# Kernel tuning notes

Hardware: AMD Instinct MI355X
Metric: run time of the kernel (lower is better)

## Reference

```python
import math
import jax, jax.numpy as jnp
import numpy as np

jax.config.update("jax_enable_x64", True)  # original module computes attention in float64

MIN_NORM = 1e-08
B, S, G = 2, 2048, 16
D_MODEL, NHEAD = 512, 8
KDIM, VDIM = 512, 512
EK, EV = KDIM // NHEAD, VDIM // NHEAD
PARAM_SCALE = 0.02  # keep exp() in range; torch.randn params at this width would overflow exp


def setup_inputs() -> dict:
    key = jax.random.key(0)
    ks = jax.random.split(key, 9)
    f32 = jnp.float32
    return {
        "query": jax.random.normal(ks[0], (B, S, D_MODEL), f32),
        "key": jax.random.normal(ks[1], (B, S, D_MODEL), f32),
        "value": jax.random.normal(ks[2], (B, S, D_MODEL), f32),
        "context": jax.random.normal(ks[3], (B, G, D_MODEL), f32),
        "query_proj": jax.random.normal(ks[4], (1, D_MODEL, KDIM), f32) * PARAM_SCALE,
        "key_proj": jax.random.normal(ks[5], (1, D_MODEL, KDIM), f32) * PARAM_SCALE,
        "value_proj": jax.random.normal(ks[6], (1, D_MODEL, VDIM), f32) * PARAM_SCALE,
        "output_proj": jax.random.normal(ks[7], (1, VDIM, D_MODEL), f32) * PARAM_SCALE,
        "context_proj": jax.random.normal(ks[8], (1, D_MODEL, KDIM), f32) * PARAM_SCALE,
    }


def _causal_attention(queries, keys, values_list):
    # queries: (B,H,G,Ek) context heads; keys: (B,H,S,Ek); values: (B,H,S,Ev)
    q = queries.astype(jnp.float64)
    k = keys.astype(jnp.float64)
    d = k.shape[-1]
    w = jnp.einsum("bhge,bhse->bhgs", q, k) / math.sqrt(d)
    w = jnp.exp(w - jnp.mean(w))            # global mean, as in original
    norms = jnp.cumsum(w, axis=-1)          # (B,H,G,S)
    norms = jnp.where(norms <= MIN_NORM, MIN_NORM, norms)
    out = []
    for v in values_list:
        v = v.astype(jnp.float64)
        # (B,H,G,S,Ev) broadcast outer product, then causal prefix-sum over S
        wv = w[..., None] * v[..., None, :, :]
        rm = jnp.cumsum(wv, axis=-2) / norms[..., None]
        out.append(jnp.swapaxes(rm, -3, -2).astype(jnp.float32))  # (B,H,S,G,Ev)
    return out


def _forward(query, key, value, context, query_proj, key_proj, value_proj, output_proj, context_proj):
    Bb, L, E = query.shape
    Gg = context.shape[1]
    H, Ek, Ev = NHEAD, KDIM // NHEAD, VDIM // NHEAD
    cs = jnp.swapaxes((context @ context_proj).reshape(Bb, Gg, H, Ek), 1, 2)  # (B,H,G,Ek)
    qs = jnp.swapaxes((query @ query_proj).reshape(Bb, L, H, Ek), 1, 2)      # (B,H,S,Ek)
    kk = jnp.swapaxes((key @ key_proj).reshape(Bb, L, H, Ek), 1, 2)          # (B,H,S,Ek)
    vs = jnp.swapaxes((value @ value_proj).reshape(Bb, L, H, Ev), 1, 2)      # (B,H,S,Ev)
    rvm, rkm = _causal_attention(cs, kk, [vs, kk])  # (B,H,S,G,Ev), (B,H,S,G,Ek)
    weights = jnp.einsum("bhse,bhsge->bhsg", qs, rkm)
    weights = jax.nn.softmax(weights, axis=-1)
    out = jnp.einsum("bhsg,bhsge->bhse", weights, rvm)      # (B,H,S,Ev)
    out = jnp.swapaxes(out, 1, 2).reshape(Bb, L, H * Ev)    # (B,S,vdim)
    return out @ output_proj                                 # (B,S,d_model)


def reference(query, key, value, context, query_proj, key_proj, value_proj, output_proj, context_proj):
    return _forward(query, key, value, context, query_proj, key_proj, value_proj, output_proj, context_proj)
```

## Files before the change

kernel.cpp:

```cpp
#include <hip/hip_runtime.h>
#include <hip/hip_bf16.h>

#define BB 2
#define SS 2048
#define GG 16
#define HH 8
#define EE 64
#define DD 512
#define NCHUNK 32
#define CLEN 64
#define CS_STRIDE 132

typedef __attribute__((ext_vector_type(8))) short bf16x8;
typedef __attribute__((ext_vector_type(4))) short s16x4;
typedef __attribute__((ext_vector_type(4))) float f32x4;

static __device__ __forceinline__ short f2bf(float x) {
  union { float f; unsigned u; } v; v.f = x;
  unsigned r = v.u + 0x7fffu + ((v.u >> 16) & 1u);
  return (short)(r >> 16);
}
static __device__ __forceinline__ float bf2f(short s) {
  return __uint_as_float(((unsigned)(unsigned short)s) << 16);
}
static __device__ __forceinline__ void bsplit(float x, short& hi, short& lo) {
  hi = f2bf(x);
  lo = f2bf(x - bf2f(hi));
}

__global__ __launch_bounds__(256) void prep_kernel(const float* __restrict__ w0,
                                                   const float* __restrict__ w1,
                                                   const float* __restrict__ w2,
                                                   const float* __restrict__ w3,
                                                   short* __restrict__ o0,
                                                   short* __restrict__ o1,
                                                   short* __restrict__ o2,
                                                   short* __restrict__ o3,
                                                   const float* __restrict__ ctxA,
                                                   const float* __restrict__ ctxW,
                                                   float* __restrict__ part,
                                                   const float* __restrict__ qin,
                                                   const float* __restrict__ kin,
                                                   const float* __restrict__ vin,
                                                   short* __restrict__ Qb,
                                                   short* __restrict__ Kb,
                                                   short* __restrict__ Vb) {
  __shared__ float smem[32 * 68 + 64 * 68];
  const int tx = threadIdx.x, ty = threadIdx.y;
  const int tid = ty * 32 + tx;
  if (blockIdx.z < 4) {
    const float* W; short* O;
    if (blockIdx.z == 0)      { W = w0; O = o0; }
    else if (blockIdx.z == 1) { W = w1; O = o1; }
    else if (blockIdx.z == 2) { W = w2; O = o2; }
    else                      { W = w3; O = o3; }
    float (*t)[33] = (float (*)[33])smem;
    const int k0 = blockIdx.x * 32, n0 = blockIdx.y * 32;
#pragma unroll
    for (int i = 0; i < 4; ++i)
      t[ty + i * 8][tx] = W[(size_t)(k0 + ty + i * 8) * DD + n0 + tx];
    __syncthreads();
#pragma unroll
    for (int i = 0; i < 4; ++i)
      O[(size_t)(n0 + ty + i * 8) * DD + k0 + tx] = f2bf(t[tx][ty + i * 8]);
    return;
  }
  if (blockIdx.z >= 5) {
    const float* src; short* dst;
    if (blockIdx.z == 5)      { src = qin; dst = Qb; }
    else if (blockIdx.z == 6) { src = kin; dst = Kb; }
    else                      { src = vin; dst = Vb; }
    const size_t base0 = (size_t)(blockIdx.y * 16 + blockIdx.x) * 8192 + tid * 8;
#pragma unroll
    for (int i = 0; i < 4; ++i) {
      size_t base = base0 + (size_t)i * 2048;
      float4 x0 = *(const float4*)(src + base);
      float4 x1 = *(const float4*)(src + base + 4);
      bf16x8 o;
      o[0] = f2bf(x0.x); o[1] = f2bf(x0.y); o[2] = f2bf(x0.z); o[3] = f2bf(x0.w);
      o[4] = f2bf(x1.x); o[5] = f2bf(x1.y); o[6] = f2bf(x1.z); o[7] = f2bf(x1.w);
      *(bf16x8*)(dst + base) = o;
    }
    return;
  }
  if (blockIdx.x >= 8 || blockIdx.y >= 8) return;
  const int nt = blockIdx.x, ky = blockIdx.y;
  float (*As)[68] = (float (*)[68])smem;
  float (*Ws)[68] = (float (*)[68])(smem + 32 * 68);
  {
    int m = tid >> 3, kq = (tid & 7) * 8;
    float4 a0 = *(const float4*)(ctxA + (size_t)m * DD + ky * 64 + kq);
    float4 a1 = *(const float4*)(ctxA + (size_t)m * DD + ky * 64 + kq + 4);
    As[m][kq + 0] = a0.x; As[m][kq + 1] = a0.y; As[m][kq + 2] = a0.z; As[m][kq + 3] = a0.w;
    As[m][kq + 4] = a1.x; As[m][kq + 5] = a1.y; As[m][kq + 6] = a1.z; As[m][kq + 7] = a1.w;
  }
  {
    int k = tid >> 2, nq = (tid & 3) * 16;
#pragma unroll
    for (int i = 0; i < 4; ++i) {
      float4 wv = *(const float4*)(ctxW + (size_t)(ky * 64 + k) * DD + nt * 64 + nq + i * 4);
      Ws[k][nq + i * 4 + 0] = wv.x; Ws[k][nq + i * 4 + 1] = wv.y;
      Ws[k][nq + i * 4 + 2] = wv.z; Ws[k][nq + i * 4 + 3] = wv.w;
    }
  }
  __syncthreads();
  const int txl = tid & 63, my = tid >> 6;
  float acc[8] = {};
  for (int k = 0; k < 64; ++k) {
    float wv = Ws[k][txl];
#pragma unroll
    for (int m = 0; m < 8; ++m) acc[m] += As[my * 8 + m][k] * wv;
  }
#pragma unroll
  for (int m = 0; m < 8; ++m)
    part[((size_t)ky * 32 + my * 8 + m) * DD + nt * 64 + txl] = acc[m];
}

#define LDA 72

__global__ __launch_bounds__(256) void proj_gemm(const short* __restrict__ a0,
                                                 const short* __restrict__ a1,
                                                 const short* __restrict__ a2,
                                                 const short* __restrict__ b0,
                                                 const short* __restrict__ b1,
                                                 const short* __restrict__ b2,
                                                 short* __restrict__ h0,
                                                 short* __restrict__ l0,
                                                 short* __restrict__ h1,
                                                 short* __restrict__ l1,
                                                 short* __restrict__ h2) {
  const short* A; const short* Bt; short* Chi; short* Clo;
  if (blockIdx.z == 0)      { A = a0; Bt = b0; Chi = h0; Clo = l0; }
  else if (blockIdx.z == 1) { A = a1; Bt = b1; Chi = h1; Clo = l1; }
  else                      { A = a2; Bt = b2; Chi = h2; Clo = nullptr; }
  const int N = DD, K = DD;
  __shared__ short As[64 * LDA];
  __shared__ short Bs[128 * LDA];
  const int tid = threadIdx.x;
  const int m0 = blockIdx.y * 64, n0 = blockIdx.x * 128;
  const int wv = tid >> 6, lane = tid & 63;
  const int wm = wv * 16;
  const int r = lane & 15, q = lane >> 4;
  f32x4 acc[8] = {};
  for (int k0 = 0; k0 < K; k0 += 64) {
    bf16x8 av[2], bvv[4];
#pragma unroll
    for (int it = 0; it < 2; ++it) {
      int idx = tid + it * 256;
      int row = idx >> 3, colq = (idx & 7) * 8;
      av[it] = *(const bf16x8*)(A + (size_t)(m0 + row) * K + k0 + colq);
    }
#pragma unroll
    for (int it = 0; it < 4; ++it) {
      int idx = tid + it * 256;
      int row = idx >> 3, colq = (idx & 7) * 8;
      bvv[it] = *(const bf16x8*)(Bt + (size_t)(n0 + row) * K + k0 + colq);
    }
    __syncthreads();
#pragma unroll
    for (int it = 0; it < 2; ++it) {
      int idx = tid + it * 256;
      int row = idx >> 3, colq = (idx & 7) * 8;
      *(bf16x8*)(&As[row * LDA + colq]) = av[it];
    }
#pragma unroll
    for (int it = 0; it < 4; ++it) {
      int idx = tid + it * 256;
      int row = idx >> 3, colq = (idx & 7) * 8;
      *(bf16x8*)(&Bs[row * LDA + colq]) = bvv[it];
    }
    __syncthreads();
#pragma unroll
    for (int ks = 0; ks < 2; ++ks) {
      bf16x8 a0r = *(const bf16x8*)(&As[(wm + r) * LDA + ks * 32 + q * 8]);
#pragma unroll
      for (int j = 0; j < 8; ++j) {
        bf16x8 br = *(const bf16x8*)(&Bs[(j * 16 + r) * LDA + ks * 32 + q * 8]);
        acc[j] = __builtin_amdgcn_mfma_f32_16x16x32_bf16(a0r, br, acc[j], 0, 0, 0);
      }
    }
  }
#pragma unroll
  for (int j = 0; j < 8; ++j)
#pragma unroll
    for (int reg = 0; reg < 4; ++reg) {
      int m = m0 + wm + q * 4 + reg;
      int n = n0 + j * 16 + r;
      float x = acc[j][reg];
      short hi = f2bf(x);
      Chi[(size_t)m * N + n] = hi;
      if (Clo) Clo[(size_t)m * N + n] = f2bf(x - bf2f(hi));
    }
}

__global__ __launch_bounds__(256) void gemm_bf16(const short* __restrict__ A,
                                                 const short* __restrict__ Bt,
                                                 float* __restrict__ C,
                                                 int M, int N, int K) {
  __shared__ short As[64 * LDA];
  __shared__ short Bs[128 * LDA];
  const int tid = threadIdx.x;
  const int m0 = blockIdx.y * 64, n0 = blockIdx.x * 128;
  const int wv = tid >> 6, lane = tid & 63;
  const int wm = wv * 16;
  const int r = lane & 15, q = lane >> 4;
  f32x4 acc[8] = {};
  for (int k0 = 0; k0 < K; k0 += 64) {
    bf16x8 av[2], bvv[4];
#pragma unroll
    for (int it = 0; it < 2; ++it) {
      int idx = tid + it * 256;
      int row = idx >> 3, colq = (idx & 7) * 8;
      av[it] = *(const bf16x8*)(A + (size_t)(m0 + row) * K + k0 + colq);
    }
#pragma unroll
    for (int it = 0; it < 4; ++it) {
      int idx = tid + it * 256;
      int row = idx >> 3, colq = (idx & 7) * 8;
      bvv[it] = *(const bf16x8*)(Bt + (size_t)(n0 + row) * K + k0 + colq);
    }
    __syncthreads();
#pragma unroll
    for (int it = 0; it < 2; ++it) {
      int idx = tid + it * 256;
      int row = idx >> 3, colq = (idx & 7) * 8;
      *(bf16x8*)(&As[row * LDA + colq]) = av[it];
    }
#pragma unroll
    for (int it = 0; it < 4; ++it) {
      int idx = tid + it * 256;
      int row = idx >> 3, colq = (idx & 7) * 8;
      *(bf16x8*)(&Bs[row * LDA + colq]) = bvv[it];
    }
    __syncthreads();
#pragma unroll
    for (int ks = 0; ks < 2; ++ks) {
      bf16x8 a0r = *(const bf16x8*)(&As[(wm + r) * LDA + ks * 32 + q * 8]);
#pragma unroll
      for (int j = 0; j < 8; ++j) {
        bf16x8 br = *(const bf16x8*)(&Bs[(j * 16 + r) * LDA + ks * 32 + q * 8]);
        acc[j] = __builtin_amdgcn_mfma_f32_16x16x32_bf16(a0r, br, acc[j], 0, 0, 0);
      }
    }
  }
#pragma unroll
  for (int j = 0; j < 8; ++j)
#pragma unroll
    for (int reg = 0; reg < 4; ++reg) {
      int m = m0 + wm + q * 4 + reg;
      int n = n0 + j * 16 + r;
      C[(size_t)m * N + n] = acc[j][reg];
    }
}

#define LDW 72
#define LDN 40

__global__ __launch_bounds__(256) void scanA_kernel(const short* __restrict__ Kh,
                                                    const short* __restrict__ Kl,
                                                    const short* __restrict__ Vb,
                                                    const float* __restrict__ part,
                                                    float* __restrict__ csums,
                                                    short* __restrict__ wG) {
  const int bh = blockIdx.y, c = blockIdx.x;
  const int b = bh >> 3, h = bh & 7;
  const int tid = threadIdx.x;
  const int lane = tid & 63, wvid = tid >> 6;
  const int r = lane & 15, q = lane >> 4;

  __shared__ short csh[16 * LDW], csl[16 * LDW];
  __shared__ short kh[64 * LDW], kl[64 * LDW];
  __shared__ short kTh[64 * LDW], kTl[64 * LDW];
  __shared__ short vT[64 * LDW];
  __shared__ short wh[16 * LDW], wl[16 * LDW];
  __shared__ float nPart[4][16];

  const int row = tid >> 2, c16 = (tid & 3) * 16;
  const size_t gb = ((size_t)(b * SS + c * CLEN + row)) * DD + h * EE + c16;
  bf16x8 kh0 = *(const bf16x8*)(Kh + gb);
  bf16x8 kh1 = *(const bf16x8*)(Kh + gb + 8);
  bf16x8 kl0 = *(const bf16x8*)(Kl + gb);
  bf16x8 kl1 = *(const bf16x8*)(Kl + gb + 8);
  bf16x8 v0 = *(const bf16x8*)(Vb + gb);
  bf16x8 v1 = *(const bf16x8*)(Vb + gb + 8);
  *(bf16x8*)(&kh[row * LDW + c16]) = kh0;
  *(bf16x8*)(&kh[row * LDW + c16 + 8]) = kh1;
  *(bf16x8*)(&kl[row * LDW + c16]) = kl0;
  *(bf16x8*)(&kl[row * LDW + c16 + 8]) = kl1;
#pragma unroll
  for (int t = 0; t < 8; ++t) {
    kTh[(c16 + t) * LDW + row] = kh0[t];
    kTh[(c16 + 8 + t) * LDW + row] = kh1[t];
    kTl[(c16 + t) * LDW + row] = kl0[t];
    kTl[(c16 + 8 + t) * LDW + row] = kl1[t];
    vT[(c16 + t) * LDW + row] = v0[t];
    vT[(c16 + 8 + t) * LDW + row] = v1[t];
  }
  {
    const int g0 = tid >> 4, t4 = (tid & 15) * 4;
    float4 csv = make_float4(0, 0, 0, 0);
#pragma unroll
    for (int ky = 0; ky < 8; ++ky) {
      float4 p = *(const float4*)(part + ((size_t)(ky * 32 + b * GG + g0)) * DD + h * EE + t4);
      csv.x += p.x; csv.y += p.y; csv.z += p.z; csv.w += p.w;
    }
    const float* pc = (const float*)&csv;
#pragma unroll
    for (int e = 0; e < 4; ++e) {
      short hi, lo;
      bsplit(pc[e], hi, lo);
      csh[g0 * LDW + t4 + e] = hi;
      csl[g0 * LDW + t4 + e] = lo;
    }
  }
  __syncthreads();

  f32x4 accw = {0.f, 0.f, 0.f, 0.f};
#pragma unroll
  for (int ks = 0; ks < 2; ++ks) {
    bf16x8 ah = *(const bf16x8*)(&csh[r * LDW + ks * 32 + q * 8]);
    bf16x8 al = *(const bf16x8*)(&csl[r * LDW + ks * 32 + q * 8]);
    bf16x8 bh = *(const bf16x8*)(&kh[(wvid * 16 + r) * LDW + ks * 32 + q * 8]);
    bf16x8 bl = *(const bf16x8*)(&kl[(wvid * 16 + r) * LDW + ks * 32 + q * 8]);
    accw = __builtin_amdgcn_mfma_f32_16x16x32_bf16(ah, bh, accw, 0, 0, 0);
    accw = __builtin_amdgcn_mfma_f32_16x16x32_bf16(ah, bl, accw, 0, 0, 0);
    accw = __builtin_amdgcn_mfma_f32_16x16x32_bf16(al, bh, accw, 0, 0, 0);
  }
  const size_t wbase = (size_t)(bh * NCHUNK + c) * 2048;
  float wf[4];
#pragma unroll
  for (int reg = 0; reg < 4; ++reg) {
    wf[reg] = expf(accw[reg] * 0.125f);
    short hi, lo;
    bsplit(wf[reg], hi, lo);
    int g = q * 4 + reg, t = wvid * 16 + r;
    wh[g * LDW + t] = hi;
    wl[g * LDW + t] = lo;
    wG[wbase + g * 64 + t] = hi;
    wG[wbase + 1024 + g * 64 + t] = lo;
  }
#pragma unroll
  for (int reg = 0; reg < 4; ++reg) {
    float np = wf[reg];
    np += __shfl_xor(np, 1);
    np += __shfl_xor(np, 2);
    np += __shfl_xor(np, 4);
    np += __shfl_xor(np, 8);
    if (r == 0) nPart[wvid][q * 4 + reg] = np;
  }
  __syncthreads();

  f32x4 ask = {0.f, 0.f, 0.f, 0.f}, asv = ask;
#pragma unroll
  for (int ks = 0; ks < 2; ++ks) {
    bf16x8 awh = *(const bf16x8*)(&wh[r * LDW + ks * 32 + q * 8]);
    bf16x8 awl = *(const bf16x8*)(&wl[r * LDW + ks * 32 + q * 8]);
    bf16x8 bkh = *(const bf16x8*)(&kTh[(wvid * 16 + r) * LDW + ks * 32 + q * 8]);
    bf16x8 bkl = *(const bf16x8*)(&kTl[(wvid * 16 + r) * LDW + ks * 32 + q * 8]);
    bf16x8 bv = *(const bf16x8*)(&vT[(wvid * 16 + r) * LDW + ks * 32 + q * 8]);
    ask = __builtin_amdgcn_mfma_f32_16x16x32_bf16(awh, bkh, ask, 0, 0, 0);
    ask = __builtin_amdgcn_mfma_f32_16x16x32_bf16(awh, bkl, ask, 0, 0, 0);
    ask = __builtin_amdgcn_mfma_f32_16x16x32_bf16(awl, bkh, ask, 0, 0, 0);
    asv = __builtin_amdgcn_mfma_f32_16x16x32_bf16(awh, bv, asv, 0, 0, 0);
    asv = __builtin_amdgcn_mfma_f32_16x16x32_bf16(awl, bv, asv, 0, 0, 0);
  }
#pragma unroll
  for (int reg = 0; reg < 4; ++reg) {
    int g = q * 4 + reg, e = wvid * 16 + r;
    size_t ob = ((size_t)((bh * NCHUNK + c) * GG + g)) * CS_STRIDE;
    csums[ob + e] = ask[reg];
    csums[ob + 64 + e] = asv[reg];
  }
  if (tid < 16) {
    size_t ob = ((size_t)((bh * NCHUNK + c) * GG + tid)) * CS_STRIDE;
    csums[ob + 128] = nPart[0][tid] + nPart[1][tid] + nPart[2][tid] + nPart[3][tid];
  }
}

__global__ __launch_bounds__(256) void chunk_kernel(const short* __restrict__ Kh,
                                                    const short* __restrict__ Vb,
                                                    const short* __restrict__ Qh,
                                                    const short* __restrict__ Ql,
                                                    const short* __restrict__ wG,
                                                    const float* __restrict__ csums,
                                                    short* __restrict__ attnbf) {
  const int c = blockIdx.x, bh = blockIdx.y;
  const int b = bh >> 3, h = bh & 7;
  const int tid = threadIdx.x;
  const int lane = tid & 63, wvid = tid >> 6;
  const int r = lane & 15, q = lane >> 4;
  const int sw = wvid * 16;

  __shared__ short qh[64 * LDW], qlo[64 * LDW], khb[64 * LDW], dh[64 * LDW];
  __shared__ short whb[16 * LDW], wlb[16 * LDW], skph[16 * LDW], skpl[16 * LDW];
  __shared__ short svpt[64 * LDN];
  __shared__ float nL[16 * 68];
  __shared__ float npreL[16];
  short* wct = qh;
  short* cmb = qlo;
  short* vt = khb;
  short* uh = dh;

  const int row = tid >> 2, c16 = (tid & 3) * 16;
  const size_t gb = ((size_t)(b * SS + c * CLEN + row)) * DD + h * EE + c16;
  bf16x8 q0 = *(const bf16x8*)(Qh + gb);
  bf16x8 q1 = *(const bf16x8*)(Qh + gb + 8);
  bf16x8 ql0 = *(const bf16x8*)(Ql + gb);
  bf16x8 ql1 = *(const bf16x8*)(Ql + gb + 8);
  bf16x8 k0 = *(const bf16x8*)(Kh + gb);
  bf16x8 k1 = *(const bf16x8*)(Kh + gb + 8);
  bf16x8 v0 = *(const bf16x8*)(Vb + gb);
  bf16x8 v1 = *(const bf16x8*)(Vb + gb + 8);
  const size_t wbase = (size_t)(bh * NCHUNK + c) * 2048;
  s16x4 wh4 = *(const s16x4*)(wG + wbase + tid * 4);
  s16x4 wl4 = *(const s16x4*)(wG + wbase + 1024 + tid * 4);

  const int g0 = tid >> 4, t4 = (tid & 15) * 4;
  float4 skv = make_float4(0, 0, 0, 0), svv = make_float4(0, 0, 0, 0);
  {
    int c2 = 0;
    for (; c2 + 4 <= c; c2 += 4) {
#pragma unroll
      for (int u = 0; u < 4; ++u) {
        size_t ob2 = ((size_t)((bh * NCHUNK + c2 + u) * GG + g0)) * CS_STRIDE;
        float4 a = *(const float4*)(csums + ob2 + t4);
        float4 bsum = *(const float4*)(csums + ob2 + 64 + t4);
        skv.x += a.x; skv.y += a.y; skv.z += a.z; skv.w += a.w;
        svv.x += bsum.x; svv.y += bsum.y; svv.z += bsum.z; svv.w += bsum.w;
      }
    }
    for (; c2 < c; ++c2) {
      size_t ob2 = ((size_t)((bh * NCHUNK + c2) * GG + g0)) * CS_STRIDE;
      float4 a = *(const float4*)(csums + ob2 + t4);
      float4 bsum = *(const float4*)(csums + ob2 + 64 + t4);
      skv.x += a.x; skv.y += a.y; skv.z += a.z; skv.w += a.w;
      svv.x += bsum.x; svv.y += bsum.y; svv.z += bsum.z; svv.w += bsum.w;
    }
  }
  if (tid < 16) {
    float npr = 0.f;
    for (int c2 = 0; c2 < c; ++c2)
      npr += csums[((size_t)((bh * NCHUNK + c2) * GG + tid)) * CS_STRIDE + 128];
    npreL[tid] = npr;
  }

  *(bf16x8*)(&qh[row * LDW + c16]) = q0;
  *(bf16x8*)(&qh[row * LDW + c16 + 8]) = q1;
  *(bf16x8*)(&qlo[row * LDW + c16]) = ql0;
  *(bf16x8*)(&qlo[row * LDW + c16 + 8]) = ql1;
  *(bf16x8*)(&khb[row * LDW + c16]) = k0;
  *(bf16x8*)(&khb[row * LDW + c16 + 8]) = k1;
  {
    int gI = (tid * 4) >> 6, tI = (tid * 4) & 63;
    *(s16x4*)(&whb[gI * LDW + tI]) = wh4;
    *(s16x4*)(&wlb[gI * LDW + tI]) = wl4;
  }
  {
    const float* ps = (const float*)&skv;
#pragma unroll
    for (int e = 0; e < 4; ++e) {
      short hi, lo;
      bsplit(ps[e], hi, lo);
      skph[g0 * LDW + t4 + e] = hi;
      skpl[g0 * LDW + t4 + e] = lo;
    }
  }
  __syncthreads();

#pragma unroll
  for (int gg = 0; gg < 4; ++gg) {
    int g = wvid * 4 + gg;
    float val = bf2f(whb[g * LDW + lane]) + bf2f(wlb[g * LDW + lane]);
#pragma unroll
    for (int d = 1; d < 64; d <<= 1) {
      float tup = __shfl_up(val, d);
      if (lane >= d) val += tup;
    }
    nL[g * 68 + lane] = npreL[g] + val;
  }

  f32x4 accd[4];
  f32x4 accwt = {0.f, 0.f, 0.f, 0.f};
#pragma unroll
  for (int ct = 0; ct < 4; ++ct) accd[ct] = accwt;
#pragma unroll
  for (int kst = 0; kst < 2; ++kst) {
    bf16x8 aq = *(const bf16x8*)(&qh[(sw + r) * LDW + kst * 32 + q * 8]);
    bf16x8 aql = *(const bf16x8*)(&qlo[(sw + r) * LDW + kst * 32 + q * 8]);
    bf16x8 bsh = *(const bf16x8*)(&skph[r * LDW + kst * 32 + q * 8]);
    bf16x8 bsl = *(const bf16x8*)(&skpl[r * LDW + kst * 32 + q * 8]);
    accwt = __builtin_amdgcn_mfma_f32_16x16x32_bf16(aq, bsh, accwt, 0, 0, 0);
    accwt = __builtin_amdgcn_mfma_f32_16x16x32_bf16(aq, bsl, accwt, 0, 0, 0);
    accwt = __builtin_amdgcn_mfma_f32_16x16x32_bf16(aql, bsh, accwt, 0, 0, 0);
#pragma unroll
    for (int ct = 0; ct < 4; ++ct) {
      bf16x8 bk = *(const bf16x8*)(&khb[(ct * 16 + r) * LDW + kst * 32 + q * 8]);
      accd[ct] = __builtin_amdgcn_mfma_f32_16x16x32_bf16(aq, bk, accd[ct], 0, 0, 0);
    }
  }
#pragma unroll
  for (int ct = 0; ct < 4; ++ct)
#pragma unroll
    for (int reg = 0; reg < 4; ++reg) {
      int sl = sw + q * 4 + reg, tl = ct * 16 + r;
      float v = (tl <= sl) ? accd[ct][reg] : 0.f;
      dh[sl * LDW + tl] = f2bf(v);
    }
  __syncthreads();

#pragma unroll
  for (int t = 0; t < 8; ++t) {
    vt[(c16 + t) * LDW + row] = v0[t];
    vt[(c16 + 8 + t) * LDW + row] = v1[t];
  }
  {
    const float* pv = (const float*)&svv;
#pragma unroll
    for (int e = 0; e < 4; ++e)
      svpt[(t4 + e) * LDN + g0] = f2bf(pv[e]);
    int ez = tid >> 2, gz = 16 + (tid & 3) * 4;
#pragma unroll
    for (int e = 0; e < 4; ++e) svpt[ez * LDN + gz + e] = 0;
    int tt = tid >> 2, gw = (tid & 3) * 4;
#pragma unroll
    for (int e = 0; e < 4; ++e) {
      wct[tt * LDN + gw + e] = whb[(gw + e) * LDW + tt];
      wct[tt * LDN + 16 + gw + e] = 0;
    }
  }

#pragma unroll
  for (int kst = 0; kst < 2; ++kst) {
    bf16x8 ad = *(const bf16x8*)(&dh[(sw + r) * LDW + kst * 32 + q * 8]);
    bf16x8 bw = *(const bf16x8*)(&whb[r * LDW + kst * 32 + q * 8]);
    bf16x8 bl = *(const bf16x8*)(&wlb[r * LDW + kst * 32 + q * 8]);
    accwt = __builtin_amdgcn_mfma_f32_16x16x32_bf16(ad, bw, accwt, 0, 0, 0);
    accwt = __builtin_amdgcn_mfma_f32_16x16x32_bf16(ad, bl, accwt, 0, 0, 0);
  }
#pragma unroll
  for (int reg = 0; reg < 4; ++reg) {
    int sl = sw + q * 4 + reg;
    float nv = fmaxf(nL[r * 68 + sl], 1e-8f);
    float wt = accwt[reg] / nv;
    float m = wt;
    m = fmaxf(m, __shfl_xor(m, 1));
    m = fmaxf(m, __shfl_xor(m, 2));
    m = fmaxf(m, __shfl_xor(m, 4));
    m = fmaxf(m, __shfl_xor(m, 8));
    float ex = expf(wt - m);
    float den = ex;
    den += __shfl_xor(den, 1);
    den += __shfl_xor(den, 2);
    den += __shfl_xor(den, 4);
    den += __shfl_xor(den, 8);
    float cmv = (ex / den) / nv;
    cmb[sl * LDN + r] = f2bf(cmv);
    cmb[sl * LDN + 16 + r] = 0;
  }
  __syncthreads();

  bf16x8 acm = *(const bf16x8*)(&cmb[(sw + r) * LDN + q * 8]);
  f32x4 accu[4];
#pragma unroll
  for (int ct = 0; ct < 4; ++ct) accu[ct] = (f32x4){0.f, 0.f, 0.f, 0.f};
#pragma unroll
  for (int ct = 0; ct < 4; ++ct) {
    bf16x8 bwc = *(const bf16x8*)(&wct[(ct * 16 + r) * LDN + q * 8]);
    accu[ct] = __builtin_amdgcn_mfma_f32_16x16x32_bf16(acm, bwc, accu[ct], 0, 0, 0);
  }
#pragma unroll
  for (int ct = 0; ct < 4; ++ct)
#pragma unroll
    for (int reg = 0; reg < 4; ++reg) {
      int sl = sw + q * 4 + reg, tl = ct * 16 + r;
      float v = (tl <= sl) ? accu[ct][reg] : 0.f;
      uh[sl * LDW + tl] = f2bf(v);
    }

  f32x4 acco[4];
#pragma unroll
  for (int et = 0; et < 4; ++et) acco[et] = (f32x4){0.f, 0.f, 0.f, 0.f};
#pragma unroll
  for (int et = 0; et < 4; ++et) {
    bf16x8 bs = *(const bf16x8*)(&svpt[(et * 16 + r) * LDN + q * 8]);
    acco[et] = __builtin_amdgcn_mfma_f32_16x16x32_bf16(acm, bs, acco[et], 0, 0, 0);
  }
#pragma unroll
  for (int kst = 0; kst < 2; ++kst) {
    bf16x8 au = *(const bf16x8*)(&uh[(sw + r) * LDW + kst * 32 + q * 8]);
#pragma unroll
    for (int et = 0; et < 4; ++et) {
      bf16x8 bv = *(const bf16x8*)(&vt[(et * 16 + r) * LDW + kst * 32 + q * 8]);
      acco[et] = __builtin_amdgcn_mfma_f32_16x16x32_bf16(au, bv, acco[et], 0, 0, 0);
    }
  }
#pragma unroll
  for (int et = 0; et < 4; ++et)
#pragma unroll
    for (int reg = 0; reg < 4; ++reg) {
      int sl = sw + q * 4 + reg;
      attnbf[((size_t)(b * SS + c * CLEN + sl)) * DD + h * EE + et * 16 + r] =
          f2bf(acco[et][reg]);
    }
}

extern "C" void kernel_launch(void* const* d_in, const int* in_sizes, int n_in,
                              void* d_out, int out_size, void* d_ws, size_t ws_size,
                              hipStream_t stream) {
  const float* query = (const float*)d_in[0];
  const float* key = (const float*)d_in[1];
  const float* value = (const float*)d_in[2];
  const float* context = (const float*)d_in[3];
  const float* query_proj = (const float*)d_in[4];
  const float* key_proj = (const float*)d_in[5];
  const float* value_proj = (const float*)d_in[6];
  const float* output_proj = (const float*)d_in[7];
  const float* context_proj = (const float*)d_in[8];
  float* out = (float*)d_out;

  const size_t MS = (size_t)BB * SS * DD;
  const size_t CSN = (size_t)BB * HH * NCHUNK * GG * CS_STRIDE;
  float* fbase = (float*)d_ws;
  float* csums = fbase;
  float* part = csums + CSN;
  short* Qh = (short*)(part + (size_t)8 * 32 * DD);
  short* Ql = Qh + MS;
  short* Kh = Ql + MS;
  short* Kl = Kh + MS;
  short* Vb = Kl + MS;
  short* Abf = Vb + MS;
  short* Wq = Abf + MS;
  short* Wk = Wq + (size_t)DD * DD;
  short* Wv = Wk + (size_t)DD * DD;
  short* Wo = Wv + (size_t)DD * DD;
  short* Qbin = Wo + (size_t)DD * DD;
  short* Kbin = Qbin + MS;
  short* Vbin = Kbin + MS;
  short* wGp = Vbin + MS;

  dim3 blk(256);
  dim3 tb(32, 8);

  prep_kernel<<<dim3(16, 16, 8), tb, 0, stream>>>(
      query_proj, key_proj, value_proj, output_proj, Wq, Wk, Wv, Wo,
      context, context_proj, part, query, key, value, Qbin, Kbin, Vbin);

  proj_gemm<<<dim3(DD / 128, (BB * SS) / 64, 3), blk, 0, stream>>>(
      Qbin, Kbin, Vbin, Wq, Wk, Wv, Qh, Ql, Kh, Kl, Vb);

  dim3 gscan(NCHUNK, BB * HH);
  scanA_kernel<<<gscan, blk, 0, stream>>>(Kh, Kl, Vb, part, csums, wGp);
  chunk_kernel<<<gscan, blk, 0, stream>>>(Kh, Vb, Qh, Ql, wGp, csums, Abf);

  gemm_bf16<<<dim3(DD / 128, (BB * SS) / 64), blk, 0, stream>>>(Abf, Wo, out, BB * SS, DD, DD);
}
```

Baseline: 140.3 us.

## Fuse chunk-sum scan and chunk attention kernels with inter-block flag synchronization

Merges the chunk-summary kernel and the per-chunk attention kernel into one launch. Each block publishes its chunk sums, sets a release flag, then spins on the flags of earlier chunks before reading prefix sums. K, V and the exp weights stay in shared memory, so the weight buffer no longer makes a round trip through global memory and one launch is dropped. This adds a memset and spin-waits that assume earlier chunks' blocks are already resident (512 blocks), and it risks stalls or deadlock if scheduling order is not guaranteed.

```diff
diff --git a/kernel.cpp b/kernel.cpp
--- a/kernel.cpp
+++ b/kernel.cpp
@@ -256,27 +256,39 @@
 #define LDW 72
 #define LDN 40
 
-__global__ __launch_bounds__(256) void scanA_kernel(const short* __restrict__ Kh,
+__global__ __launch_bounds__(256) void fused_kernel(const short* __restrict__ Kh,
                                                     const short* __restrict__ Kl,
                                                     const short* __restrict__ Vb,
+                                                    const short* __restrict__ Qg,
+                                                    const short* __restrict__ Qlg,
                                                     const float* __restrict__ part,
-                                                    float* __restrict__ csums,
-                                                    short* __restrict__ wG) {
-  const int bh = blockIdx.y, c = blockIdx.x;
+                                                    float* csums,
+                                                    unsigned int* flags,
+                                                    short* __restrict__ attnbf) {
+  const int c = blockIdx.x, bh = blockIdx.y;
   const int b = bh >> 3, h = bh & 7;
   const int tid = threadIdx.x;
   const int lane = tid & 63, wvid = tid >> 6;
   const int r = lane & 15, q = lane >> 4;
+  const int sw = wvid * 16;
 
   __shared__ short csh[16 * LDW], csl[16 * LDW];
   __shared__ short kh[64 * LDW], kl[64 * LDW];
-  __shared__ short kTh[64 * LDW], kTl[64 * LDW];
-  __shared__ short vT[64 * LDW];
+  __shared__ short kTh[64 * LDW], kTl[64 * LDW], vT[64 * LDW];
   __shared__ short wh[16 * LDW], wl[16 * LDW];
+  __shared__ short svpt[64 * LDN];
   __shared__ float nPart[4][16];
+  __shared__ float nL[16 * 68];
+  __shared__ float npreL[16];
+  short* qh = kTh;
+  short* qlo = kTl;
+  short* dh = kl;
+  short* wct = kTh;
+  short* cmb = kTl;
 
   const int row = tid >> 2, c16 = (tid & 3) * 16;
   const size_t gb = ((size_t)(b * SS + c * CLEN + row)) * DD + h * EE + c16;
+
   bf16x8 kh0 = *(const bf16x8*)(Kh + gb);
   bf16x8 kh1 = *(const bf16x8*)(Kh + gb + 8);
   bf16x8 kl0 = *(const bf16x8*)(Kl + gb);
@@ -296,8 +308,8 @@
     vT[(c16 + t) * LDW + row] = v0[t];
     vT[(c16 + 8 + t) * LDW + row] = v1[t];
   }
-  {
-    const int g0 = tid >> 4, t4 = (tid & 15) * 4;
+  const int g0 = tid >> 4, t4 = (tid & 15) * 4;
+  {
     float4 csv = make_float4(0, 0, 0, 0);
 #pragma unroll
     for (int ky = 0; ky < 8; ++ky) {
@@ -315,107 +327,84 @@
   }
   __syncthreads();
 
-  f32x4 accw = {0.f, 0.f, 0.f, 0.f};
-#pragma unroll
-  for (int ks = 0; ks < 2; ++ks) {
-    bf16x8 ah = *(const bf16x8*)(&csh[r * LDW + ks * 32 + q * 8]);
-    bf16x8 al = *(const bf16x8*)(&csl[r * LDW + ks * 32 + q * 8]);
-    bf16x8 bh = *(const bf16x8*)(&kh[(wvid * 16 + r) * LDW + ks * 32 + q * 8]);
-    bf16x8 bl = *(const bf16x8*)(&kl[(wvid * 16 + r) * LDW + ks * 32 + q * 8]);
-    accw = __builtin_amdgcn_mfma_f32_16x16x32_bf16(ah, bh, accw, 0, 0, 0);
-    accw = __builtin_amdgcn_mfma_f32_16x16x32_bf16(ah, bl, accw, 0, 0, 0);
-    accw = __builtin_amdgcn_mfma_f32_16x16x32_bf16(al, bh, accw, 0, 0, 0);
-  }
-  const size_t wbase = (size_t)(bh * NCHUNK + c) * 2048;
-  float wf[4];
-#pragma unroll
-  for (int reg = 0; reg < 4; ++reg) {
-    wf[reg] = expf(accw[reg] * 0.125f);
-    short hi, lo;
-    bsplit(wf[reg], hi, lo);
-    int g = q * 4 + reg, t = wvid * 16 + r;
-    wh[g * LDW + t] = hi;
-    wl[g * LDW + t] = lo;
-    wG[wbase + g * 64 + t] = hi;
-    wG[wbase + 1024 + g * 64 + t] = lo;
-  }
-#pragma unroll
-  for (int reg = 0; reg < 4; ++reg) {
-    float np = wf[reg];
-    np += __shfl_xor(np, 1);
-    np += __shfl_xor(np, 2);
-    np += __shfl_xor(np, 4);
-    np += __shfl_xor(np, 8);
-    if (r == 0) nPart[wvid][q * 4 + reg] = np;
-  }
-  __syncthreads();
-
-  f32x4 ask = {0.f, 0.f, 0.f, 0.f}, asv = ask;
-#pragma unroll
-  for (int ks = 0; ks < 2; ++ks) {
-    bf16x8 awh = *(const bf16x8*)(&wh[r * LDW + ks * 32 + q * 8]);
-    bf16x8 awl = *(const bf16x8*)(&wl[r * LDW + ks * 32 + q * 8]);
-    bf16x8 bkh = *(const bf16x8*)(&kTh[(wvid * 16 + r) * LDW + ks * 32 + q * 8]);
-    bf16x8 bkl = *(const bf16x8*)(&kTl[(wvid * 16 + r) * LDW + ks * 32 + q * 8]);
-    bf16x8 bv = *(const bf16x8*)(&vT[(wvid * 16 + r) * LDW + ks * 32 + q * 8]);
-    ask = __builtin_amdgcn_mfma_f32_16x16x32_bf16(awh, bkh, ask, 0, 0, 0);
-    ask = __builtin_amdgcn_mfma_f32_16x16x32_bf16(awh, bkl, ask, 0, 0, 0);
-    ask = __builtin_amdgcn_mfma_f32_16x16x32_bf16(awl, bkh, ask, 0, 0, 0);
-    asv = __builtin_amdgcn_mfma_f32_16x16x32_bf16(awh, bv, asv, 0, 0, 0);
-    asv = __builtin_amdgcn_mfma_f32_16x16x32_bf16(awl, bv, asv, 0, 0, 0);
-  }
-#pragma unroll
-  for (int reg = 0; reg < 4; ++reg) {
-    int g = q * 4 + reg, e = wvid * 16 + r;
-    size_t ob = ((size_t)((bh * NCHUNK + c) * GG + g)) * CS_STRIDE;
-    csums[ob + e] = ask[reg];
-    csums[ob + 64 + e] = asv[reg];
-  }
-  if (tid < 16) {
-    size_t ob = ((size_t)((bh * NCHUNK + c) * GG + tid)) * CS_STRIDE;
-    csums[ob + 128] = nPart[0][tid] + nPart[1][tid] + nPart[2][tid] + nPart[3][tid];
-  }
-}
-
-__global__ __launch_bounds__(256) void chunk_kernel(const short* __restrict__ Kh,
-                                                    const short* __restrict__ Vb,
-                                                    const short* __restrict__ Qh,
-                                                    const short* __restrict__ Ql,
-                                                    const short* __restrict__ wG,
-                                                    const float* __restrict__ csums,
-                                                    short* __restrict__ attnbf) {
-  const int c = blockIdx.x, bh = blockIdx.y;
-  const int b = bh >> 3, h = bh & 7;
-  const int tid = threadIdx.x;
-  const int lane = tid & 63, wvid = tid >> 6;
-  const int r = lane & 15, q = lane >> 4;
-  const int sw = wvid * 16;
-
-  __shared__ short qh[64 * LDW], qlo[64 * LDW], khb[64 * LDW], dh[64 * LDW];
-  __shared__ short whb[16 * LDW], wlb[16 * LDW], skph[16 * LDW], skpl[16 * LDW];
-  __shared__ short svpt[64 * LDN];
-  __shared__ float nL[16 * 68];
-  __shared__ float npreL[16];
-  short* wct = qh;
-  short* cmb = qlo;
-  short* vt = khb;
-  short* uh = dh;
-
-  const int row = tid >> 2, c16 = (tid & 3) * 16;
-  const size_t gb = ((size_t)(b * SS + c * CLEN + row)) * DD + h * EE + c16;
-  bf16x8 q0 = *(const bf16x8*)(Qh + gb);
-  bf16x8 q1 = *(const bf16x8*)(Qh + gb + 8);
-  bf16x8 ql0 = *(const bf16x8*)(Ql + gb);
-  bf16x8 ql1 = *(const bf16x8*)(Ql + gb + 8);
-  bf16x8 k0 = *(const bf16x8*)(Kh + gb);
-  bf16x8 k1 = *(const bf16x8*)(Kh + gb + 8);
-  bf16x8 v0 = *(const bf16x8*)(Vb + gb);
-  bf16x8 v1 = *(const bf16x8*)(Vb + gb + 8);
-  const size_t wbase = (size_t)(bh * NCHUNK + c) * 2048;
-  s16x4 wh4 = *(const s16x4*)(wG + wbase + tid * 4);
-  s16x4 wl4 = *(const s16x4*)(wG + wbase + 1024 + tid * 4);
-
-  const int g0 = tid >> 4, t4 = (tid & 15) * 4;
+  {
+    f32x4 accw = {0.f, 0.f, 0.f, 0.f};
+#pragma unroll
+    for (int ks = 0; ks < 2; ++ks) {
+      bf16x8 ah = *(const bf16x8*)(&csh[r * LDW + ks * 32 + q * 8]);
+      bf16x8 al = *(const bf16x8*)(&csl[r * LDW + ks * 32 + q * 8]);
+      bf16x8 bh = *(const bf16x8*)(&kh[(wvid * 16 + r) * LDW + ks * 32 + q * 8]);
+      bf16x8 bl = *(const bf16x8*)(&kl[(wvid * 16 + r) * LDW + ks * 32 + q * 8]);
+      accw = __builtin_amdgcn_mfma_f32_16x16x32_bf16(ah, bh, accw, 0, 0, 0);
+      accw = __builtin_amdgcn_mfma_f32_16x16x32_bf16(ah, bl, accw, 0, 0, 0);
+      accw = __builtin_amdgcn_mfma_f32_16x16x32_bf16(al, bh, accw, 0, 0, 0);
+    }
+    float wf[4];
+#pragma unroll
+    for (int reg = 0; reg < 4; ++reg) {
+      wf[reg] = expf(accw[reg] * 0.125f);
+      short hi, lo;
+      bsplit(wf[reg], hi, lo);
+      int g = q * 4 + reg, t = wvid * 16 + r;
+      wh[g * LDW + t] = hi;
+      wl[g * LDW + t] = lo;
+    }
+#pragma unroll
+    for (int reg = 0; reg < 4; ++reg) {
+      float np = wf[reg];
+      np += __shfl_xor(np, 1);
+      np += __shfl_xor(np, 2);
+      np += __shfl_xor(np, 4);
+      np += __shfl_xor(np, 8);
+      if (r == 0) nPart[wvid][q * 4 + reg] = np;
+    }
+  }
+  __syncthreads();
+
+  {
+    f32x4 ask = {0.f, 0.f, 0.f, 0.f}, asv = ask;
+#pragma unroll
+    for (int ks = 0; ks < 2; ++ks) {
+      bf16x8 awh = *(const bf16x8*)(&wh[r * LDW + ks * 32 + q * 8]);
+      bf16x8 awl = *(const bf16x8*)(&wl[r * LDW + ks * 32 + q * 8]);
+      bf16x8 bkh = *(const bf16x8*)(&kTh[(wvid * 16 + r) * LDW + ks * 32 + q * 8]);
+      bf16x8 bkl = *(const bf16x8*)(&kTl[(wvid * 16 + r) * LDW + ks * 32 + q * 8]);
+      bf16x8 bv = *(const bf16x8*)(&vT[(wvid * 16 + r) * LDW + ks * 32 + q * 8]);
+      ask = __builtin_amdgcn_mfma_f32_16x16x32_bf16(awh, bkh, ask, 0, 0, 0);
+      ask = __builtin_amdgcn_mfma_f32_16x16x32_bf16(awh, bkl, ask, 0, 0, 0);
+      ask = __builtin_amdgcn_mfma_f32_16x16x32_bf16(awl, bkh, ask, 0, 0, 0);
+      asv = __builtin_amdgcn_mfma_f32_16x16x32_bf16(awh, bv, asv, 0, 0, 0);
+      asv = __builtin_amdgcn_mfma_f32_16x16x32_bf16(awl, bv, asv, 0, 0, 0);
+    }
+#pragma unroll
+    for (int reg = 0; reg < 4; ++reg) {
+      int g = q * 4 + reg, e = wvid * 16 + r;
+      size_t ob = ((size_t)((bh * NCHUNK + c) * GG + g)) * CS_STRIDE;
+      csums[ob + e] = ask[reg];
+      csums[ob + 64 + e] = asv[reg];
+    }
+    if (tid < 16) {
+      size_t ob = ((size_t)((bh * NCHUNK + c) * GG + tid)) * CS_STRIDE;
+      csums[ob + 128] = nPart[0][tid] + nPart[1][tid] + nPart[2][tid] + nPart[3][tid];
+    }
+  }
+
+  __threadfence();
+  __syncthreads();
+  if (tid == 0)
+    __hip_atomic_store(&flags[bh * NCHUNK + c], 1u, __ATOMIC_RELEASE,
+                       __HIP_MEMORY_SCOPE_AGENT);
+  if (tid < c) {
+    while (__hip_atomic_load(&flags[bh * NCHUNK + tid], __ATOMIC_ACQUIRE,
+                             __HIP_MEMORY_SCOPE_AGENT) == 0u) {}
+  }
+  __syncthreads();
+
+  bf16x8 q0 = *(const bf16x8*)(Qg + gb);
+  bf16x8 q1 = *(const bf16x8*)(Qg + gb + 8);
+  bf16x8 ql0 = *(const bf16x8*)(Qlg + gb);
+  bf16x8 ql1 = *(const bf16x8*)(Qlg + gb + 8);
+
   float4 skv = make_float4(0, 0, 0, 0), svv = make_float4(0, 0, 0, 0);
   {
     int c2 = 0;
@@ -448,21 +437,14 @@
   *(bf16x8*)(&qh[row * LDW + c16 + 8]) = q1;
   *(bf16x8*)(&qlo[row * LDW + c16]) = ql0;
   *(bf16x8*)(&qlo[row * LDW + c16 + 8]) = ql1;
-  *(bf16x8*)(&khb[row * LDW + c16]) = k0;
-  *(bf16x8*)(&khb[row * LDW + c16 + 8]) = k1;
-  {
-    int gI = (tid * 4) >> 6, tI = (tid * 4) & 63;
-    *(s16x4*)(&whb[gI * LDW + tI]) = wh4;
-    *(s16x4*)(&wlb[gI * LDW + tI]) = wl4;
-  }
   {
     const float* ps = (const float*)&skv;
 #pragma unroll
     for (int e = 0; e < 4; ++e) {
       short hi, lo;
       bsplit(ps[e], hi, lo);
-      skph[g0 * LDW + t4 + e] = hi;
-      skpl[g0 * LDW + t4 + e] = lo;
+      csh[g0 * LDW + t4 + e] = hi;
+      csl[g0 * LDW + t4 + e] = lo;
     }
   }
   __syncthreads();
@@ -470,7 +452,7 @@
 #pragma unroll
   for (int gg = 0; gg < 4; ++gg) {
     int g = wvid * 4 + gg;
-    float val = bf2f(whb[g * LDW + lane]) + bf2f(wlb[g * LDW + lane]);
+    float val = bf2f(wh[g * LDW + lane]) + bf2f(wl[g * LDW + lane]);
 #pragma unroll
     for (int d = 1; d < 64; d <<= 1) {
       float tup = __shfl_up(val, d);
@@ -487,14 +469,14 @@
   for (int kst = 0; kst < 2; ++kst) {
     bf16x8 aq = *(const bf16x8*)(&qh[(sw + r) * LDW + kst * 32 + q * 8]);
     bf16x8 aql = *(const bf16x8*)(&qlo[(sw + r) * LDW + kst * 32 + q * 8]);
-    bf16x8 bsh = *(const bf16x8*)(&skph[r * LDW + kst * 32 + q * 8]);
-    bf16x8 bsl = *(const bf16x8*)(&skpl[r * LDW + kst * 32 + q * 8]);
+    bf16x8 bsh = *(const bf16x8*)(&csh[r * LDW + kst * 32 + q * 8]);
+    bf16x8 bsl = *(const bf16x8*)(&csl[r * LDW + kst * 32 + q * 8]);
     accwt = __builtin_amdgcn_mfma_f32_16x16x32_bf16(aq, bsh, accwt, 0, 0, 0);
     accwt = __builtin_amdgcn_mfma_f32_16x16x32_bf16(aq, bsl, accwt, 0, 0, 0);
     accwt = __builtin_amdgcn_mfma_f32_16x16x32_bf16(aql, bsh, accwt, 0, 0, 0);
 #pragma unroll
     for (int ct = 0; ct < 4; ++ct) {
-      bf16x8 bk = *(const bf16x8*)(&khb[(ct * 16 + r) * LDW + kst * 32 + q * 8]);
+      bf16x8 bk = *(const bf16x8*)(&kh[(ct * 16 + r) * LDW + kst * 32 + q * 8]);
       accd[ct] = __builtin_amdgcn_mfma_f32_16x16x32_bf16(aq, bk, accd[ct], 0, 0, 0);
     }
   }
@@ -508,11 +490,6 @@
     }
   __syncthreads();
 
-#pragma unroll
-  for (int t = 0; t < 8; ++t) {
-    vt[(c16 + t) * LDW + row] = v0[t];
-    vt[(c16 + 8 + t) * LDW + row] = v1[t];
-  }
   {
     const float* pv = (const float*)&svv;
 #pragma unroll
@@ -524,7 +501,7 @@
     int tt = tid >> 2, gw = (tid & 3) * 4;
 #pragma unroll
     for (int e = 0; e < 4; ++e) {
-      wct[tt * LDN + gw + e] = whb[(gw + e) * LDW + tt];
+      wct[tt * LDN + gw + e] = wh[(gw + e) * LDW + tt];
       wct[tt * LDN + 16 + gw + e] = 0;
     }
   }
@@ -532,8 +509,8 @@
 #pragma unroll
   for (int kst = 0; kst < 2; ++kst) {
     bf16x8 ad = *(const bf16x8*)(&dh[(sw + r) * LDW + kst * 32 + q * 8]);
-    bf16x8 bw = *(const bf16x8*)(&whb[r * LDW + kst * 32 + q * 8]);
-    bf16x8 bl = *(const bf16x8*)(&wlb[r * LDW + kst * 32 + q * 8]);
+    bf16x8 bw = *(const bf16x8*)(&wh[r * LDW + kst * 32 + q * 8]);
+    bf16x8 bl = *(const bf16x8*)(&wl[r * LDW + kst * 32 + q * 8]);
     accwt = __builtin_amdgcn_mfma_f32_16x16x32_bf16(ad, bw, accwt, 0, 0, 0);
     accwt = __builtin_amdgcn_mfma_f32_16x16x32_bf16(ad, bl, accwt, 0, 0, 0);
   }
@@ -574,7 +551,7 @@
     for (int reg = 0; reg < 4; ++reg) {
       int sl = sw + q * 4 + reg, tl = ct * 16 + r;
       float v = (tl <= sl) ? accu[ct][reg] : 0.f;
-      uh[sl * LDW + tl] = f2bf(v);
+      dh[sl * LDW + tl] = f2bf(v);
     }
 
   f32x4 acco[4];
@@ -587,10 +564,10 @@
   }
 #pragma unroll
   for (int kst = 0; kst < 2; ++kst) {
-    bf16x8 au = *(const bf16x8*)(&uh[(sw + r) * LDW + kst * 32 + q * 8]);
+    bf16x8 au = *(const bf16x8*)(&dh[(sw + r) * LDW + kst * 32 + q * 8]);
 #pragma unroll
     for (int et = 0; et < 4; ++et) {
-      bf16x8 bv = *(const bf16x8*)(&vt[(et * 16 + r) * LDW + kst * 32 + q * 8]);
+      bf16x8 bv = *(const bf16x8*)(&vT[(et * 16 + r) * LDW + kst * 32 + q * 8]);
       acco[et] = __builtin_amdgcn_mfma_f32_16x16x32_bf16(au, bv, acco[et], 0, 0, 0);
     }
   }
@@ -636,10 +613,12 @@
   short* Qbin = Wo + (size_t)DD * DD;
   short* Kbin = Qbin + MS;
   short* Vbin = Kbin + MS;
-  short* wGp = Vbin + MS;
+  unsigned int* flags = (unsigned int*)(Vbin + MS);
 
   dim3 blk(256);
   dim3 tb(32, 8);
+
+  hipMemsetAsync(flags, 0, (size_t)BB * HH * NCHUNK * sizeof(unsigned int), stream);
 
   prep_kernel<<<dim3(16, 16, 8), tb, 0, stream>>>(
       query_proj, key_proj, value_proj, output_proj, Wq, Wk, Wv, Wo,
@@ -649,8 +628,7 @@
       Qbin, Kbin, Vbin, Wq, Wk, Wv, Qh, Ql, Kh, Kl, Vb);
 
   dim3 gscan(NCHUNK, BB * HH);
-  scanA_kernel<<<gscan, blk, 0, stream>>>(Kh, Kl, Vb, part, csums, wGp);
-  chunk_kernel<<<gscan, blk, 0, stream>>>(Kh, Vb, Qh, Ql, wGp, csums, Abf);
+  fused_kernel<<<gscan, blk, 0, stream>>>(Kh, Kl, Vb, Qh, Ql, part, csums, flags, Abf);
 
   gemm_bf16<<<dim3(DD / 128, (BB * SS) / 64), blk, 0, stream>>>(Abf, Wo, out, BB * SS, DD, DD);
 }
```

After: 205.2 us. +46.2%, slower.
